# Performance work log

Hardware: AMD Instinct MI355X
Metric: run time of the kernel (lower is better)

The kernel has to match this reference:

```python
import jax, jax.numpy as jnp
import numpy as np

N_NODES = 100000
N_EDGES = 1600000
N_GRAPHS = 128
IN_F, H_F, OUT_F, HID, NCLS = 128, 128, 64, 10, 10

def setup_inputs() -> dict:
    key = jax.random.key(0)
    ks = jax.random.split(key, 12)
    feats = jax.random.normal(ks[0], (N_NODES, IN_F), dtype=jnp.float32)
    src = jax.random.randint(ks[1], (N_EDGES,), 0, N_NODES, dtype=jnp.int32)
    dst = jax.random.randint(ks[2], (N_EDGES,), 0, N_NODES, dtype=jnp.int32)
    graph_ids = jnp.sort(jax.random.randint(ks[3], (N_NODES,), 0, N_GRAPHS, dtype=jnp.int32))
    def glorot(k, shape):
        fan = shape[0] + shape[1]
        return jax.random.normal(k, shape, dtype=jnp.float32) * jnp.sqrt(2.0 / fan)
    return {
        'feats': feats, 'src': src, 'dst': dst, 'graph_ids': graph_ids,
        'W1': glorot(ks[4], (IN_F, H_F)), 'b1': jnp.zeros((H_F,), jnp.float32),
        'W2': glorot(ks[5], (H_F, OUT_F)), 'b2': jnp.zeros((OUT_F,), jnp.float32),
        'fcW1': glorot(ks[6], (OUT_F, HID)), 'fcb1': jnp.zeros((HID,), jnp.float32),
        'fcW2': glorot(ks[7], (HID, NCLS)), 'fcb2': jnp.zeros((NCLS,), jnp.float32),
    }

def _graph_conv(x, W, b, src, dst):
    # DGL GraphConv, norm='both': D_dst^{-1/2} A D_src^{-1/2} X W + b
    ones = jnp.ones((src.shape[0],), x.dtype)
    deg_out = jnp.clip(jax.ops.segment_sum(ones, src, num_segments=N_NODES), 1.0)
    deg_in = jnp.clip(jax.ops.segment_sum(ones, dst, num_segments=N_NODES), 1.0)
    x = x * jax.lax.rsqrt(deg_out)[:, None]
    m = jax.ops.segment_sum(x[src], dst, num_segments=N_NODES)  # gather-scatter over edges
    m = m * jax.lax.rsqrt(deg_in)[:, None]
    return m @ W + b

def reference(feats, src, dst, graph_ids, W1, b1, W2, b2, fcW1, fcb1, fcW2, fcb2):
    h = jax.nn.relu(_graph_conv(feats, W1, b1, src, dst))
    h = jax.nn.relu(_graph_conv(h, W2, b2, src, dst))
    # dgl.mean_nodes: per-graph mean pooling
    sums = jax.ops.segment_sum(h, graph_ids, num_segments=N_GRAPHS)
    counts = jnp.clip(jax.ops.segment_sum(jnp.ones((N_NODES,), h.dtype), graph_ids, num_segments=N_GRAPHS), 1.0)
    pooled = sums / counts[:, None]  # [G, OUT_F]
    z = jax.nn.relu(pooled @ fcW1 + fcb1)
    return jax.nn.softmax(z @ fcW2 + fcb2, axis=1)
```

## Files before the change

kernel.cpp:

```cpp
#include <hip/hip_runtime.h>
#include <hip/hip_bf16.h>

#define N_NODES 100000
#define N_EDGES 1600000
#define N_GRAPHS 128
#define IN_F 128
#define H_F 128
#define OUT_F 64
#define HID 10
#define NCLS 10
#define XPAD 136
#define BSH 7
#define NBUCK 782
#define SBLK 128
#define EPB (N_EDGES / SBLK)
#define NB_PREP 4
#define PCHUNK 8

typedef __attribute__((ext_vector_type(8))) short bf16x8;
typedef __attribute__((ext_vector_type(4))) float f32x4;
typedef __attribute__((ext_vector_type(2))) float f32x2;

__device__ __forceinline__ float bl(unsigned int u) { return __uint_as_float(u << 16); }
__device__ __forceinline__ float bh(unsigned int u) { return __uint_as_float(u & 0xffff0000u); }

__global__ __launch_bounds__(256) void k_zero(int* __restrict__ p, int n) {
    int i = blockIdx.x * 256 + threadIdx.x;
    int stride = gridDim.x * 256;
    for (; i < n; i += stride) p[i] = 0;
}

__global__ __launch_bounds__(1024) void k_hist2(const int* __restrict__ src, const int* __restrict__ dst,
                                                int* __restrict__ Pd, int* __restrict__ cnt_out,
                                                const float* __restrict__ W1, const float* __restrict__ W2,
                                                unsigned short* __restrict__ Wt1, unsigned short* __restrict__ Wt2) {
    __shared__ int hd[NBUCK];
    const int blk = blockIdx.x;
    if (blk < SBLK) {
        for (int i = threadIdx.x; i < NBUCK; i += 1024) hd[i] = 0;
        __syncthreads();
        const int base = blk * EPB;
        for (int i = threadIdx.x; i < EPB; i += 1024) {
            atomicAdd(&hd[dst[base + i] >> BSH], 1);
            atomicAdd(&cnt_out[src[base + i]], 1);
        }
        __syncthreads();
        for (int b = threadIdx.x; b < NBUCK; b += 1024) Pd[b * SBLK + blk] = hd[b];
    } else {
        int t = (blk - SBLK) * 1024 + threadIdx.x;
        const int stride = NB_PREP * 1024;
        for (int i = t; i < 128 * 128; i += stride) {
            int c = i >> 7, k = i & 127;
            __hip_bfloat16 v = __float2bfloat16(W1[k * 128 + c]);
            Wt1[i] = *(unsigned short*)&v;
        }
        for (int i = t; i < 64 * 128; i += stride) {
            int c = i >> 7, k = i & 127;
            __hip_bfloat16 v = __float2bfloat16(W2[k * 64 + c]);
            Wt2[i] = *(unsigned short*)&v;
        }
    }
}

__global__ __launch_bounds__(128) void k_scanA(int* __restrict__ Pd, int* __restrict__ Td) {
    __shared__ int sc[128];
    const int b = blockIdx.x;
    const int t = threadIdx.x;
    int v = Pd[b * SBLK + t];
    sc[t] = v;
    __syncthreads();
    for (int off = 1; off < 128; off <<= 1) {
        int u = (t >= off) ? sc[t - off] : 0;
        __syncthreads();
        sc[t] += u;
        __syncthreads();
    }
    Pd[b * SBLK + t] = sc[t] - v;
    if (t == 127) Td[b] = sc[127];
}

__global__ __launch_bounds__(1024) void k_scanB(const int* __restrict__ Td, int* __restrict__ Bd) {
    __shared__ int sc[1024];
    const int t = threadIdx.x;
    int v = (t < NBUCK) ? Td[t] : 0;
    sc[t] = v;
    __syncthreads();
    for (int off = 1; off < 1024; off <<= 1) {
        int u = (t >= off) ? sc[t - off] : 0;
        __syncthreads();
        sc[t] += u;
        __syncthreads();
    }
    if (t < NBUCK) Bd[t] = sc[t] - v;
    if (t == NBUCK - 1) Bd[NBUCK] = sc[t];
}

__global__ __launch_bounds__(1024) void k_scatter(const int* __restrict__ src, const int* __restrict__ dst,
                                                  const int* __restrict__ Pd, const int* __restrict__ Bd,
                                                  unsigned int* __restrict__ pb) {
    __shared__ int tk[NBUCK];
    const int blk = blockIdx.x;
    for (int i = threadIdx.x; i < NBUCK; i += 1024) tk[i] = 0;
    __syncthreads();
    const int base = blk * EPB;
    for (int i = threadIdx.x; i < EPB; i += 1024) {
        int d = dst[base + i];
        int s = src[base + i];
        int bd = d >> BSH;
        int t = atomicAdd(&tk[bd], 1);
        pb[Bd[bd] + Pd[bd * SBLK + blk] + t] = ((unsigned)s << 7) | (unsigned)(d & 127);
    }
}

__global__ __launch_bounds__(256) void k_finalize(const unsigned int* __restrict__ pb, const int* __restrict__ Bd,
                                                  int* __restrict__ rp, int* __restrict__ cols) {
    __shared__ int cnt[128];
    __shared__ int exc[128];
    __shared__ int tick[128];
    __shared__ int sc[128];
    const int b = blockIdx.x;
    const int tid = threadIdx.x;
    if (tid < 128) { cnt[tid] = 0; tick[tid] = 0; }
    __syncthreads();
    const int e0 = Bd[b], e1 = Bd[b + 1];
    for (int i = e0 + tid; i < e1; i += 256) atomicAdd(&cnt[pb[i] & 127], 1);
    __syncthreads();
    if (tid < 128) sc[tid] = cnt[tid];
    __syncthreads();
    for (int off = 1; off < 128; off <<= 1) {
        int u = (tid < 128 && tid >= off) ? sc[tid - off] : 0;
        __syncthreads();
        if (tid < 128) sc[tid] += u;
        __syncthreads();
    }
    if (tid < 128) exc[tid] = sc[tid] - cnt[tid];
    __syncthreads();
    const int node0 = b << BSH;
    if (tid < 128 && node0 + tid < N_NODES) rp[node0 + tid] = e0 + exc[tid];
    if (b == NBUCK - 1 && tid == 0) rp[N_NODES] = N_EDGES;
    for (int i = e0 + tid; i < e1; i += 256) {
        unsigned int p = pb[i];
        int loc = p & 127;
        int t = atomicAdd(&tick[loc], 1);
        cols[e0 + exc[loc] + t] = (int)(p >> 7);
    }
}

__global__ __launch_bounds__(256) void k_gemm1(const float* __restrict__ X,
                                               const unsigned short* __restrict__ Wt,
                                               const int* __restrict__ cnt_out,
                                               unsigned char* __restrict__ Gout) {
    __shared__ __align__(16) unsigned short Xs[32 * XPAD];
    __shared__ __align__(16) unsigned short Ws[128 * XPAD];
    const int tid = threadIdx.x;
    const int row0 = blockIdx.x * 32;

    {
        const float4* X4 = (const float4*)X;
#pragma unroll
        for (int j = 0; j < 4; j++) {
            int i = tid + 256 * j;
            int r = i >> 5, k4 = i & 31;
            float4 x = X4[(size_t)(row0 + r) * 32 + k4];
            __hip_bfloat162 lo = __float22bfloat162_rn({x.x, x.y});
            __hip_bfloat162 hi = __float22bfloat162_rn({x.z, x.w});
            uint2 u;
            u.x = *(unsigned int*)&lo;
            u.y = *(unsigned int*)&hi;
            *(uint2*)&Xs[r * XPAD + k4 * 4] = u;
        }
    }
    {
        const uint2* W2 = (const uint2*)Wt;
#pragma unroll
        for (int j = 0; j < 16; j++) {
            int i = tid + 256 * j;
            int cc = i >> 5, kk = i & 31;
            uint2 u = W2[(size_t)cc * 32 + kk];
            *(uint2*)&Ws[cc * XPAD + kk * 4] = u;
        }
    }
    __syncthreads();

    const int lane = tid & 63;
    const int wv = tid >> 6;
    const int m = lane & 15;
    const int q = lane >> 4;
    const int cg = wv * 32;

    f32x4 acc00 = {0.f, 0.f, 0.f, 0.f}, acc01 = {0.f, 0.f, 0.f, 0.f};
    f32x4 acc10 = {0.f, 0.f, 0.f, 0.f}, acc11 = {0.f, 0.f, 0.f, 0.f};
#pragma unroll
    for (int ks = 0; ks < 4; ks++) {
        int kb = ks * 32 + q * 8;
        bf16x8 a0 = *(const bf16x8*)&Xs[m * XPAD + kb];
        bf16x8 a1 = *(const bf16x8*)&Xs[(16 + m) * XPAD + kb];
        bf16x8 b0 = *(const bf16x8*)&Ws[(cg + m) * XPAD + kb];
        bf16x8 b1 = *(const bf16x8*)&Ws[(cg + 16 + m) * XPAD + kb];
        acc00 = __builtin_amdgcn_mfma_f32_16x16x32_bf16(a0, b0, acc00, 0, 0, 0);
        acc01 = __builtin_amdgcn_mfma_f32_16x16x32_bf16(a0, b1, acc01, 0, 0, 0);
        acc10 = __builtin_amdgcn_mfma_f32_16x16x32_bf16(a1, b0, acc10, 0, 0, 0);
        acc11 = __builtin_amdgcn_mfma_f32_16x16x32_bf16(a1, b1, acc11, 0, 0, 0);
    }
#pragma unroll
    for (int r = 0; r < 4; r++) {
        int rowA = row0 + q * 4 + r;
        int rowB = rowA + 16;
        float sA = rsqrtf((float)max(cnt_out[rowA], 1));
        float sB = rsqrtf((float)max(cnt_out[rowB], 1));
        unsigned int pkA = __builtin_amdgcn_cvt_pk_fp8_f32(acc00[r] * sA, acc01[r] * sA, 0, false);
        unsigned int pkB = __builtin_amdgcn_cvt_pk_fp8_f32(acc10[r] * sB, acc11[r] * sB, 0, false);
        unsigned char* gA = Gout + (size_t)rowA * 128 + cg + m;
        gA[0]  = (unsigned char)(pkA & 0xffu);
        gA[16] = (unsigned char)((pkA >> 8) & 0xffu);
        unsigned char* gB = Gout + (size_t)rowB * 128 + cg + m;
        gB[0]  = (unsigned char)(pkB & 0xffu);
        gB[16] = (unsigned char)((pkB >> 8) & 0xffu);
    }
}

template <int TOTF, bool XBF16, bool OUT_FP8>
__global__ __launch_bounds__(256) void k_gemm_mfma(const void* __restrict__ Xv,
                                                   const unsigned short* __restrict__ Wt,
                                                   const int* __restrict__ cnt_out,
                                                   void* __restrict__ GoutV) {
    __shared__ __align__(16) unsigned short Xs[32 * XPAD];
    __shared__ __align__(16) unsigned short Ws[64 * XPAD];
    const int tid = threadIdx.x;
    const int cbase = blockIdx.y * 64;
    const int row0 = blockIdx.x * 32;

    if constexpr (XBF16) {
        const uint2* X2 = (const uint2*)Xv;
#pragma unroll
        for (int j = 0; j < 4; j++) {
            int i = tid + 256 * j;
            int r = i >> 5, kk = i & 31;
            uint2 u = X2[(size_t)(row0 + r) * 32 + kk];
            *(uint2*)&Xs[r * XPAD + kk * 4] = u;
        }
    } else {
        const float4* X4 = (const float4*)Xv;
#pragma unroll
        for (int j = 0; j < 4; j++) {
            int i = tid + 256 * j;
            int r = i >> 5, k4 = i & 31;
            float4 x = X4[(size_t)(row0 + r) * 32 + k4];
            __hip_bfloat162 lo = __float22bfloat162_rn({x.x, x.y});
            __hip_bfloat162 hi = __float22bfloat162_rn({x.z, x.w});
            uint2 u;
            u.x = *(unsigned int*)&lo;
            u.y = *(unsigned int*)&hi;
            *(uint2*)&Xs[r * XPAD + k4 * 4] = u;
        }
    }
    {
        const uint2* W2 = (const uint2*)Wt;
#pragma unroll
        for (int j = 0; j < 8; j++) {
            int i = tid + 256 * j;
            int c = i >> 5, kk = i & 31;
            uint2 u = W2[(size_t)(cbase + c) * 32 + kk];
            *(uint2*)&Ws[c * XPAD + kk * 4] = u;
        }
    }
    __syncthreads();

    const int lane = tid & 63;
    const int wv = tid >> 6;
    const int m = lane & 15;
    const int q = lane >> 4;
    const int roff = (wv & 1) * 16;
    const int coff = (wv >> 1) * 32;

    f32x4 acc0 = {0.f, 0.f, 0.f, 0.f}, acc1 = {0.f, 0.f, 0.f, 0.f};
#pragma unroll
    for (int ks = 0; ks < 4; ks++) {
        int kb = ks * 32 + q * 8;
        bf16x8 a  = *(const bf16x8*)&Xs[(roff + m) * XPAD + kb];
        bf16x8 b0 = *(const bf16x8*)&Ws[(coff + m) * XPAD + kb];
        bf16x8 b1 = *(const bf16x8*)&Ws[(coff + 16 + m) * XPAD + kb];
        acc0 = __builtin_amdgcn_mfma_f32_16x16x32_bf16(a, b0, acc0, 0, 0, 0);
        acc1 = __builtin_amdgcn_mfma_f32_16x16x32_bf16(a, b1, acc1, 0, 0, 0);
    }
#pragma unroll
    for (int r = 0; r < 4; r++) {
        int row = row0 + roff + q * 4 + r;
        float s = rsqrtf((float)max(cnt_out[row], 1));
        int col0 = cbase + coff + m;
        if constexpr (OUT_FP8) {
            unsigned int pk = __builtin_amdgcn_cvt_pk_fp8_f32(acc0[r] * s, acc1[r] * s, 0, false);
            unsigned char* gp = (unsigned char*)GoutV + (size_t)row * TOTF + col0;
            gp[0]  = (unsigned char)(pk & 0xffu);
            gp[16] = (unsigned char)((pk >> 8) & 0xffu);
        } else {
            unsigned short* Gout = (unsigned short*)GoutV;
            __hip_bfloat16 o0 = __float2bfloat16(acc0[r] * s);
            __hip_bfloat16 o1 = __float2bfloat16(acc1[r] * s);
            Gout[(size_t)row * TOTF + col0]      = *(unsigned short*)&o0;
            Gout[(size_t)row * TOTF + col0 + 16] = *(unsigned short*)&o1;
        }
    }
}

__device__ __forceinline__ void tail128(const unsigned short* __restrict__ gl, const int* __restrict__ cols,
                                        int b, int d, int j, f32x2& acc) {
    while (j + 16 <= d) {
        unsigned int u[16];
#pragma unroll
        for (int k = 0; k < 16; k++) { int s = cols[b + j + k]; u[k] = gl[(size_t)s * 64]; }
#pragma unroll
        for (int k = 0; k < 16; k++) acc += __builtin_amdgcn_cvt_pk_f32_fp8(u[k], false);
        j += 16;
    }
    if (j + 8 <= d) {
        unsigned int u[8];
#pragma unroll
        for (int k = 0; k < 8; k++) { int s = cols[b + j + k]; u[k] = gl[(size_t)s * 64]; }
#pragma unroll
        for (int k = 0; k < 8; k++) acc += __builtin_amdgcn_cvt_pk_f32_fp8(u[k], false);
        j += 8;
    }
    if (j + 4 <= d) {
        unsigned int u[4];
#pragma unroll
        for (int k = 0; k < 4; k++) { int s = cols[b + j + k]; u[k] = gl[(size_t)s * 64]; }
#pragma unroll
        for (int k = 0; k < 4; k++) acc += __builtin_amdgcn_cvt_pk_f32_fp8(u[k], false);
        j += 4;
    }
    if (j + 2 <= d) {
        unsigned int u0, u1;
        { int s = cols[b + j];     u0 = gl[(size_t)s * 64]; }
        { int s = cols[b + j + 1]; u1 = gl[(size_t)s * 64]; }
        acc += __builtin_amdgcn_cvt_pk_f32_fp8(u0, false);
        acc += __builtin_amdgcn_cvt_pk_f32_fp8(u1, false);
        j += 2;
    }
    if (j < d) {
        int s = cols[b + j];
        unsigned int u = gl[(size_t)s * 64];
        acc += __builtin_amdgcn_cvt_pk_f32_fp8(u, false);
    }
}

__device__ __forceinline__ void tail64(const unsigned char* __restrict__ gl, const int* __restrict__ cols,
                                       int b, int d, int j, f32x2& acc) {
    while (j + 16 <= d) {
        unsigned int u[16];
#pragma unroll
        for (int k = 0; k < 16; k++) { int s = cols[b + j + k]; u[k] = gl[(size_t)s * 64]; }
#pragma unroll
        for (int k = 0; k < 16; k++) acc += __builtin_amdgcn_cvt_pk_f32_fp8(u[k], false);
        j += 16;
    }
    if (j + 8 <= d) {
        unsigned int u[8];
#pragma unroll
        for (int k = 0; k < 8; k++) { int s = cols[b + j + k]; u[k] = gl[(size_t)s * 64]; }
#pragma unroll
        for (int k = 0; k < 8; k++) acc += __builtin_amdgcn_cvt_pk_f32_fp8(u[k], false);
        j += 8;
    }
    if (j + 4 <= d) {
        unsigned int u[4];
#pragma unroll
        for (int k = 0; k < 4; k++) { int s = cols[b + j + k]; u[k] = gl[(size_t)s * 64]; }
#pragma unroll
        for (int k = 0; k < 4; k++) acc += __builtin_amdgcn_cvt_pk_f32_fp8(u[k], false);
        j += 4;
    }
    if (j + 2 <= d) {
        unsigned int u0, u1;
        { int s = cols[b + j];     u0 = gl[(size_t)s * 64]; }
        { int s = cols[b + j + 1]; u1 = gl[(size_t)s * 64]; }
        acc += __builtin_amdgcn_cvt_pk_f32_fp8(u0, false);
        acc += __builtin_amdgcn_cvt_pk_f32_fp8(u1, false);
        j += 2;
    }
    if (j < d) {
        int s = cols[b + j];
        unsigned int u = gl[(size_t)s * 64];
        acc += __builtin_amdgcn_cvt_pk_f32_fp8(u, false);
    }
}

__global__ __launch_bounds__(256) void k_spmm128f8(const unsigned short* __restrict__ G,
                                                   const int* __restrict__ rp,
                                                   const int* __restrict__ cols,
                                                   const float* __restrict__ bias,
                                                   unsigned int* __restrict__ H) {
    const int lane = threadIdx.x & 63;
    const int wave = threadIdx.x >> 6;
    const int v0 = (blockIdx.x * 4 + wave) * 2;
    const int b0 = __builtin_amdgcn_readfirstlane(rp[v0]);
    const int b1 = __builtin_amdgcn_readfirstlane(rp[v0 + 1]);
    const int e1 = __builtin_amdgcn_readfirstlane(rp[v0 + 2]);
    const int dA = b1 - b0, dB = e1 - b1;
    const unsigned short* gl = G + lane;
    f32x2 aA = {0.f, 0.f}, aB = {0.f, 0.f};
    int ja = 0, jb = 0;
    while (ja + 8 <= dA && jb + 8 <= dB) {
        unsigned int u[8], w[8];
#pragma unroll
        for (int k = 0; k < 8; k++) { int s = cols[b0 + ja + k]; u[k] = gl[(size_t)s * 64]; }
#pragma unroll
        for (int k = 0; k < 8; k++) { int s = cols[b1 + jb + k]; w[k] = gl[(size_t)s * 64]; }
#pragma unroll
        for (int k = 0; k < 8; k++) aA += __builtin_amdgcn_cvt_pk_f32_fp8(u[k], false);
#pragma unroll
        for (int k = 0; k < 8; k++) aB += __builtin_amdgcn_cvt_pk_f32_fp8(w[k], false);
        ja += 8; jb += 8;
    }
    tail128(gl, cols, b0, dA, ja, aA);
    tail128(gl, cols, b1, dB, jb, aB);

    {
        const float rs = rsqrtf((float)max(dA, 1));
        const float2 bb = *(const float2*)&bias[2 * lane];
        __hip_bfloat162 p = __float22bfloat162_rn({fmaxf(fmaf(aA.x, rs, bb.x), 0.f),
                                                   fmaxf(fmaf(aA.y, rs, bb.y), 0.f)});
        H[(size_t)v0 * 64 + lane] = *(unsigned int*)&p;
    }
    {
        const float rs = rsqrtf((float)max(dB, 1));
        const float2 bb = *(const float2*)&bias[2 * lane];
        __hip_bfloat162 p = __float22bfloat162_rn({fmaxf(fmaf(aB.x, rs, bb.x), 0.f),
                                                   fmaxf(fmaf(aB.y, rs, bb.y), 0.f)});
        H[(size_t)(v0 + 1) * 64 + lane] = *(unsigned int*)&p;
    }
}

__global__ __launch_bounds__(256) void k_spmm64f8(const unsigned char* __restrict__ G,
                                                  const int* __restrict__ rp,
                                                  const int* __restrict__ cols,
                                                  const float* __restrict__ bias,
                                                  unsigned short* __restrict__ H) {
    const int lane = threadIdx.x & 63;
    const int wave = threadIdx.x >> 6;
    const int v0 = (blockIdx.x * 4 + wave) * 2;
    const int b0 = __builtin_amdgcn_readfirstlane(rp[v0]);
    const int b1 = __builtin_amdgcn_readfirstlane(rp[v0 + 1]);
    const int e1 = __builtin_amdgcn_readfirstlane(rp[v0 + 2]);
    const int dA = b1 - b0, dB = e1 - b1;
    const unsigned char* gl = G + lane;
    f32x2 aA = {0.f, 0.f}, aB = {0.f, 0.f};
    int ja = 0, jb = 0;
    while (ja + 8 <= dA && jb + 8 <= dB) {
        unsigned int u[8], w[8];
#pragma unroll
        for (int k = 0; k < 8; k++) { int s = cols[b0 + ja + k]; u[k] = gl[(size_t)s * 64]; }
#pragma unroll
        for (int k = 0; k < 8; k++) { int s = cols[b1 + jb + k]; w[k] = gl[(size_t)s * 64]; }
#pragma unroll
        for (int k = 0; k < 8; k++) aA += __builtin_amdgcn_cvt_pk_f32_fp8(u[k], false);
#pragma unroll
        for (int k = 0; k < 8; k++) aB += __builtin_amdgcn_cvt_pk_f32_fp8(w[k], false);
        ja += 8; jb += 8;
    }
    tail64(gl, cols, b0, dA, ja, aA);
    tail64(gl, cols, b1, dB, jb, aB);

    {
        const float rs = rsqrtf((float)max(dA, 1));
        __hip_bfloat16 o = __float2bfloat16(fmaxf(fmaf(aA.x, rs, bias[lane]), 0.f));
        H[(size_t)v0 * 64 + lane] = *(unsigned short*)&o;
    }
    {
        const float rs = rsqrtf((float)max(dB, 1));
        __hip_bfloat16 o = __float2bfloat16(fmaxf(fmaf(aB.x, rs, bias[lane]), 0.f));
        H[(size_t)(v0 + 1) * 64 + lane] = *(unsigned short*)&o;
    }
}

__global__ __launch_bounds__(256) void k_pool(const unsigned short* __restrict__ h2,
                                              const int* __restrict__ gid,
                                              float* __restrict__ part) {
    __shared__ int se[2];
    __shared__ float red[16][16][4];
    const int cpart = blockIdx.x;
    const int g = blockIdx.y;
    const int tid = threadIdx.x;
    if (tid < 2) {
        int target = g + tid;
        int lo = 0, hi = N_NODES;
        while (lo < hi) {
            int mid = (lo + hi) >> 1;
            if (gid[mid] < target) lo = mid + 1; else hi = mid;
        }
        se[tid] = lo;
    }
    __syncthreads();
    const int s = se[0], e = se[1];
    const int chunk = (e - s + PCHUNK - 1) / PCHUNK;
    const int lo = s + cpart * chunk;
    const int hi = min(lo + chunk, e);
    const int r = tid >> 4, cp = tid & 15;
    float a0 = 0.f, a1 = 0.f, a2 = 0.f, a3 = 0.f;
    const uint2* H = (const uint2*)h2;
    for (int v = lo + r; v < hi; v += 16) {
        uint2 u = H[(size_t)v * 16 + cp];
        a0 += bl(u.x); a1 += bh(u.x); a2 += bl(u.y); a3 += bh(u.y);
    }
    red[r][cp][0] = a0; red[r][cp][1] = a1; red[r][cp][2] = a2; red[r][cp][3] = a3;
    for (int off = 8; off > 0; off >>= 1) {
        __syncthreads();
        if (r < off) {
#pragma unroll
            for (int k = 0; k < 4; k++) red[r][cp][k] += red[r + off][cp][k];
        }
    }
    __syncthreads();
    if (r == 0) {
        float4 o = {red[0][cp][0], red[0][cp][1], red[0][cp][2], red[0][cp][3]};
        *(float4*)&part[((size_t)cpart * N_GRAPHS + g) * 64 + 4 * cp] = o;
    }
}

__global__ __launch_bounds__(64) void k_mlp(const float* __restrict__ part,
                                            const int* __restrict__ gid,
                                            const float* __restrict__ fcW1,
                                            const float* __restrict__ fcb1,
                                            const float* __restrict__ fcW2,
                                            const float* __restrict__ fcb2,
                                            float* __restrict__ out) {
    __shared__ int se[2];
    __shared__ float p[64];
    __shared__ float z[10];
    __shared__ float l[10];
    __shared__ float red[2];
    const int g = blockIdx.x;
    const int t = threadIdx.x;
    if (t < 2) {
        int target = g + t;
        int lo = 0, hi = N_NODES;
        while (lo < hi) {
            int mid = (lo + hi) >> 1;
            if (gid[mid] < target) lo = mid + 1; else hi = mid;
        }
        se[t] = lo;
    }
    __syncthreads();
    const int cnt = max(se[1] - se[0], 1);
    float a = 0.f;
#pragma unroll
    for (int c = 0; c < PCHUNK; c++) a += part[((size_t)c * N_GRAPHS + g) * 64 + t];
    p[t] = a / (float)cnt;
    __syncthreads();
    if (t < 10) {
        float acc = fcb1[t];
        for (int k = 0; k < 64; k++) acc = fmaf(p[k], fcW1[k * 10 + t], acc);
        z[t] = fmaxf(acc, 0.f);
    }
    __syncthreads();
    if (t < 10) {
        float acc = fcb2[t];
        for (int k = 0; k < 10; k++) acc = fmaf(z[k], fcW2[k * 10 + t], acc);
        l[t] = acc;
    }
    __syncthreads();
    if (t == 0) {
        float m = l[0];
        for (int i = 1; i < 10; i++) m = fmaxf(m, l[i]);
        float ssum = 0.f;
        for (int i = 0; i < 10; i++) ssum += expf(l[i] - m);
        red[0] = m;
        red[1] = ssum;
    }
    __syncthreads();
    if (t < 10) out[g * 10 + t] = expf(l[t] - red[0]) / red[1];
}

extern "C" void kernel_launch(void* const* d_in, const int* in_sizes, int n_in,
                              void* d_out, int out_size, void* d_ws, size_t ws_size,
                              hipStream_t stream) {
    const float* feats = (const float*)d_in[0];
    const int* src = (const int*)d_in[1];
    const int* dst = (const int*)d_in[2];
    const int* gid = (const int*)d_in[3];
    const float* W1 = (const float*)d_in[4];
    const float* b1 = (const float*)d_in[5];
    const float* W2 = (const float*)d_in[6];
    const float* b2 = (const float*)d_in[7];
    const float* fcW1 = (const float*)d_in[8];
    const float* fcb1 = (const float*)d_in[9];
    const float* fcW2 = (const float*)d_in[10];
    const float* fcb2 = (const float*)d_in[11];
    float* out = (float*)d_out;

    char* w = (char*)d_ws;
    size_t off = 0;
    auto alloc = [&](size_t bytes) -> void* {
        void* p = w + off;
        off = (off + bytes + 255) & ~(size_t)255;
        return p;
    };
    int* cnt_out = (int*)alloc(N_NODES * 4);
    int* rp      = (int*)alloc((N_NODES + 1) * 4);
    int* cols    = (int*)alloc((size_t)N_EDGES * 4);
    int* Pd      = (int*)alloc(NBUCK * SBLK * 4);
    int* Td      = (int*)alloc(NBUCK * 4);
    int* Bd      = (int*)alloc((NBUCK + 1) * 4);
    unsigned int* pb  = (unsigned int*)alloc((size_t)N_EDGES * 4);
    unsigned short* Wt1 = (unsigned short*)alloc(128 * 128 * 2);
    unsigned short* Wt2 = (unsigned short*)alloc(64 * 128 * 2);
    unsigned char* g1 = (unsigned char*)alloc((size_t)N_NODES * 128);
    unsigned short* h1 = (unsigned short*)alloc((size_t)N_NODES * 128 * 2);
    unsigned char* g2 = (unsigned char*)alloc((size_t)N_NODES * 64);
    unsigned short* h2 = (unsigned short*)alloc((size_t)N_NODES * 64 * 2);
    float* part = (float*)alloc((size_t)PCHUNK * N_GRAPHS * 64 * 4);

    k_zero<<<256, 256, 0, stream>>>(cnt_out, N_NODES);
    k_hist2<<<SBLK + NB_PREP, 1024, 0, stream>>>(src, dst, Pd, cnt_out, W1, W2, Wt1, Wt2);
    k_scanA<<<NBUCK, 128, 0, stream>>>(Pd, Td);
    k_scanB<<<1, 1024, 0, stream>>>(Td, Bd);
    k_scatter<<<SBLK, 1024, 0, stream>>>(src, dst, Pd, Bd, pb);
    k_finalize<<<NBUCK, 256, 0, stream>>>(pb, Bd, rp, cols);

    k_gemm1<<<N_NODES / 32, 256, 0, stream>>>(feats, Wt1, cnt_out, g1);
    k_spmm128f8<<<N_NODES / 8, 256, 0, stream>>>((const unsigned short*)g1, rp, cols, b1, (unsigned int*)h1);

    k_gemm_mfma<64, true, true><<<dim3(N_NODES / 32, 1), 256, 0, stream>>>(h1, Wt2, cnt_out, g2);
    k_spmm64f8<<<N_NODES / 8, 256, 0, stream>>>(g2, rp, cols, b2, (unsigned short*)h2);

    k_pool<<<dim3(PCHUNK, N_GRAPHS), 256, 0, stream>>>(h2, gid, part);
    k_mlp<<<N_GRAPHS, 64, 0, stream>>>(part, gid, fcW1, fcb1, fcW2, fcb2, out);
}
```

Baseline: 320.5 us.

## Compute out-degrees via bucketed counting sort instead of global atomics

Replaces the per-edge global atomicAdd on cnt_out (and its zeroing kernel) with a second bucketed histogram over source ids. That histogram is scanned, scattered into a byte buffer and counted in shared memory inside the finalize kernel. This removes 1.6M contended global atomics and one launch. In exchange it adds an extra scatter pass, a second scan and a 1.6MB byte buffer write and read.

```diff
diff --git a/kernel.cpp b/kernel.cpp
--- a/kernel.cpp
+++ b/kernel.cpp
@@ -24,28 +24,26 @@
 __device__ __forceinline__ float bl(unsigned int u) { return __uint_as_float(u << 16); }
 __device__ __forceinline__ float bh(unsigned int u) { return __uint_as_float(u & 0xffff0000u); }
 
-__global__ __launch_bounds__(256) void k_zero(int* __restrict__ p, int n) {
-    int i = blockIdx.x * 256 + threadIdx.x;
-    int stride = gridDim.x * 256;
-    for (; i < n; i += stride) p[i] = 0;
-}
-
 __global__ __launch_bounds__(1024) void k_hist2(const int* __restrict__ src, const int* __restrict__ dst,
-                                                int* __restrict__ Pd, int* __restrict__ cnt_out,
+                                                int* __restrict__ Pd, int* __restrict__ Ps,
                                                 const float* __restrict__ W1, const float* __restrict__ W2,
                                                 unsigned short* __restrict__ Wt1, unsigned short* __restrict__ Wt2) {
     __shared__ int hd[NBUCK];
+    __shared__ int hs[NBUCK];
     const int blk = blockIdx.x;
     if (blk < SBLK) {
-        for (int i = threadIdx.x; i < NBUCK; i += 1024) hd[i] = 0;
+        for (int i = threadIdx.x; i < NBUCK; i += 1024) { hd[i] = 0; hs[i] = 0; }
         __syncthreads();
         const int base = blk * EPB;
         for (int i = threadIdx.x; i < EPB; i += 1024) {
             atomicAdd(&hd[dst[base + i] >> BSH], 1);
-            atomicAdd(&cnt_out[src[base + i]], 1);
-        }
-        __syncthreads();
-        for (int b = threadIdx.x; b < NBUCK; b += 1024) Pd[b * SBLK + blk] = hd[b];
+            atomicAdd(&hs[src[base + i] >> BSH], 1);
+        }
+        __syncthreads();
+        for (int b = threadIdx.x; b < NBUCK; b += 1024) {
+            Pd[b * SBLK + blk] = hd[b];
+            Ps[b * SBLK + blk] = hs[b];
+        }
     } else {
         int t = (blk - SBLK) * 1024 + threadIdx.x;
         const int stride = NB_PREP * 1024;
@@ -62,11 +60,15 @@
     }
 }
 
-__global__ __launch_bounds__(128) void k_scanA(int* __restrict__ Pd, int* __restrict__ Td) {
+__global__ __launch_bounds__(128) void k_scanA(int* __restrict__ Pd, int* __restrict__ Ps,
+                                               int* __restrict__ Td, int* __restrict__ Ts) {
     __shared__ int sc[128];
     const int b = blockIdx.x;
     const int t = threadIdx.x;
-    int v = Pd[b * SBLK + t];
+    int* P = (b < NBUCK) ? Pd : Ps;
+    int* T = (b < NBUCK) ? Td : Ts;
+    const int bb = (b < NBUCK) ? b : b - NBUCK;
+    int v = P[bb * SBLK + t];
     sc[t] = v;
     __syncthreads();
     for (int off = 1; off < 128; off <<= 1) {
@@ -75,11 +77,12 @@
         sc[t] += u;
         __syncthreads();
     }
-    Pd[b * SBLK + t] = sc[t] - v;
-    if (t == 127) Td[b] = sc[127];
-}
-
-__global__ __launch_bounds__(1024) void k_scanB(const int* __restrict__ Td, int* __restrict__ Bd) {
+    P[bb * SBLK + t] = sc[t] - v;
+    if (t == 127) T[bb] = sc[127];
+}
+
+__global__ __launch_bounds__(1024) void k_scanB(const int* __restrict__ Td, const int* __restrict__ Ts,
+                                                int* __restrict__ Bd, int* __restrict__ Bs) {
     __shared__ int sc[1024];
     const int t = threadIdx.x;
     int v = (t < NBUCK) ? Td[t] : 0;
@@ -93,37 +96,66 @@
     }
     if (t < NBUCK) Bd[t] = sc[t] - v;
     if (t == NBUCK - 1) Bd[NBUCK] = sc[t];
+    __syncthreads();
+    int v2 = (t < NBUCK) ? Ts[t] : 0;
+    sc[t] = v2;
+    __syncthreads();
+    for (int off = 1; off < 1024; off <<= 1) {
+        int u = (t >= off) ? sc[t - off] : 0;
+        __syncthreads();
+        sc[t] += u;
+        __syncthreads();
+    }
+    if (t < NBUCK) Bs[t] = sc[t] - v2;
+    if (t == NBUCK - 1) Bs[NBUCK] = sc[t];
 }
 
 __global__ __launch_bounds__(1024) void k_scatter(const int* __restrict__ src, const int* __restrict__ dst,
-                                                  const int* __restrict__ Pd, const int* __restrict__ Bd,
-                                                  unsigned int* __restrict__ pb) {
+                                                  const int* __restrict__ Pd, const int* __restrict__ Ps,
+                                                  const int* __restrict__ Bd, const int* __restrict__ Bs,
+                                                  unsigned int* __restrict__ pb, unsigned char* __restrict__ sb) {
     __shared__ int tk[NBUCK];
-    const int blk = blockIdx.x;
+    const int b = blockIdx.x;
+    const bool isPb = b < SBLK;
+    const int blk = isPb ? b : b - SBLK;
     for (int i = threadIdx.x; i < NBUCK; i += 1024) tk[i] = 0;
     __syncthreads();
     const int base = blk * EPB;
-    for (int i = threadIdx.x; i < EPB; i += 1024) {
-        int d = dst[base + i];
-        int s = src[base + i];
-        int bd = d >> BSH;
-        int t = atomicAdd(&tk[bd], 1);
-        pb[Bd[bd] + Pd[bd * SBLK + blk] + t] = ((unsigned)s << 7) | (unsigned)(d & 127);
+    if (isPb) {
+        for (int i = threadIdx.x; i < EPB; i += 1024) {
+            int d = dst[base + i];
+            int s = src[base + i];
+            int bd = d >> BSH;
+            int t = atomicAdd(&tk[bd], 1);
+            pb[Bd[bd] + Pd[bd * SBLK + blk] + t] = ((unsigned)s << 7) | (unsigned)(d & 127);
+        }
+    } else {
+        for (int i = threadIdx.x; i < EPB; i += 1024) {
+            int s = src[base + i];
+            int bs = s >> BSH;
+            int t = atomicAdd(&tk[bs], 1);
+            sb[Bs[bs] + Ps[bs * SBLK + blk] + t] = (unsigned char)(s & 127);
+        }
     }
 }
 
 __global__ __launch_bounds__(256) void k_finalize(const unsigned int* __restrict__ pb, const int* __restrict__ Bd,
-                                                  int* __restrict__ rp, int* __restrict__ cols) {
+                                                  const unsigned char* __restrict__ sb, const int* __restrict__ Bs,
+                                                  int* __restrict__ rp, int* __restrict__ cnt_out,
+                                                  int* __restrict__ cols) {
     __shared__ int cnt[128];
     __shared__ int exc[128];
     __shared__ int tick[128];
+    __shared__ int h[128];
     __shared__ int sc[128];
     const int b = blockIdx.x;
     const int tid = threadIdx.x;
-    if (tid < 128) { cnt[tid] = 0; tick[tid] = 0; }
+    if (tid < 128) { cnt[tid] = 0; tick[tid] = 0; h[tid] = 0; }
     __syncthreads();
     const int e0 = Bd[b], e1 = Bd[b + 1];
     for (int i = e0 + tid; i < e1; i += 256) atomicAdd(&cnt[pb[i] & 127], 1);
+    const int f0 = Bs[b], f1 = Bs[b + 1];
+    for (int i = f0 + tid; i < f1; i += 256) atomicAdd(&h[sb[i]], 1);
     __syncthreads();
     if (tid < 128) sc[tid] = cnt[tid];
     __syncthreads();
@@ -136,7 +168,10 @@
     if (tid < 128) exc[tid] = sc[tid] - cnt[tid];
     __syncthreads();
     const int node0 = b << BSH;
-    if (tid < 128 && node0 + tid < N_NODES) rp[node0 + tid] = e0 + exc[tid];
+    if (tid < 128 && node0 + tid < N_NODES) {
+        rp[node0 + tid] = e0 + exc[tid];
+        cnt_out[node0 + tid] = h[tid];
+    }
     if (b == NBUCK - 1 && tid == 0) rp[N_NODES] = N_EDGES;
     for (int i = e0 + tid; i < e1; i += 256) {
         unsigned int p = pb[i];
@@ -599,9 +634,13 @@
     int* rp      = (int*)alloc((N_NODES + 1) * 4);
     int* cols    = (int*)alloc((size_t)N_EDGES * 4);
     int* Pd      = (int*)alloc(NBUCK * SBLK * 4);
+    int* Ps      = (int*)alloc(NBUCK * SBLK * 4);
     int* Td      = (int*)alloc(NBUCK * 4);
+    int* Ts      = (int*)alloc(NBUCK * 4);
     int* Bd      = (int*)alloc((NBUCK + 1) * 4);
+    int* Bs      = (int*)alloc((NBUCK + 1) * 4);
     unsigned int* pb  = (unsigned int*)alloc((size_t)N_EDGES * 4);
+    unsigned char* sb = (unsigned char*)alloc((size_t)N_EDGES);
     unsigned short* Wt1 = (unsigned short*)alloc(128 * 128 * 2);
     unsigned short* Wt2 = (unsigned short*)alloc(64 * 128 * 2);
     unsigned char* g1 = (unsigned char*)alloc((size_t)N_NODES * 128);
@@ -610,12 +649,11 @@
     unsigned short* h2 = (unsigned short*)alloc((size_t)N_NODES * 64 * 2);
     float* part = (float*)alloc((size_t)PCHUNK * N_GRAPHS * 64 * 4);
 
-    k_zero<<<256, 256, 0, stream>>>(cnt_out, N_NODES);
-    k_hist2<<<SBLK + NB_PREP, 1024, 0, stream>>>(src, dst, Pd, cnt_out, W1, W2, Wt1, Wt2);
-    k_scanA<<<NBUCK, 128, 0, stream>>>(Pd, Td);
-    k_scanB<<<1, 1024, 0, stream>>>(Td, Bd);
-    k_scatter<<<SBLK, 1024, 0, stream>>>(src, dst, Pd, Bd, pb);
-    k_finalize<<<NBUCK, 256, 0, stream>>>(pb, Bd, rp, cols);
+    k_hist2<<<SBLK + NB_PREP, 1024, 0, stream>>>(src, dst, Pd, Ps, W1, W2, Wt1, Wt2);
+    k_scanA<<<2 * NBUCK, 128, 0, stream>>>(Pd, Ps, Td, Ts);
+    k_scanB<<<1, 1024, 0, stream>>>(Td, Ts, Bd, Bs);
+    k_scatter<<<2 * SBLK, 1024, 0, stream>>>(src, dst, Pd, Ps, Bd, Bs, pb, sb);
+    k_finalize<<<NBUCK, 256, 0, stream>>>(pb, Bd, sb, Bs, rp, cnt_out, cols);
 
     k_gemm1<<<N_NODES / 32, 256, 0, stream>>>(feats, Wt1, cnt_out, g1);
     k_spmm128f8<<<N_NODES / 8, 256, 0, stream>>>((const unsigned short*)g1, rp, cols, b1, (unsigned int*)h1);
```

After: 271.8 us. 15.2% less time.
